# Performance work log

Measured on AMD Instinct MI355X. Metric: run time of the kernel, lower is better.

Reference implementation:

```python
import jax, jax.numpy as jnp
import numpy as np

LATENT = 128
HEADS = 4
HEAD_DIM = LATENT // HEADS
NUM_BUCKETS = 32
MAX_DISTANCE = 100000
B, N = 8, 2048


def relative_position_bucket(qpos, kpos):
    """T5-style bidirectional relative position bucketing.
    qpos, kpos: [B, N] int -> buckets [B, N, N] int32 in [0, NUM_BUCKETS).
    """
    rel = kpos[:, None, :] - qpos[:, :, None]  # [B, Nq, Nk]
    half = NUM_BUCKETS // 2
    buckets = (rel > 0).astype(jnp.int32) * half
    arel = jnp.abs(rel)
    max_exact = half // 2
    is_small = arel < max_exact
    # log-spaced buckets for larger distances
    large = max_exact + (
        jnp.log(jnp.maximum(arel, 1).astype(jnp.float32) / max_exact)
        / np.log(MAX_DISTANCE / max_exact)
        * (half - max_exact)
    ).astype(jnp.int32)
    large = jnp.minimum(large, half - 1)
    return buckets + jnp.where(is_small, arel.astype(jnp.int32), large)


def setup_inputs() -> dict:
    key = jax.random.key(0)
    ks = jax.random.split(key, 12)
    s = 0.02
    x = jax.random.normal(ks[0], (B, N, LATENT), dtype=jnp.float32)
    positions = jnp.sort(jax.random.randint(ks[1], (B, N), 0, 1000000), axis=-1)
    mask = jnp.ones((B, N), dtype=bool)
    Wq = jax.random.normal(ks[2], (LATENT, LATENT), dtype=jnp.float32) * s
    bq = jax.random.normal(ks[3], (LATENT,), dtype=jnp.float32) * s
    Wk = jax.random.normal(ks[4], (LATENT, LATENT), dtype=jnp.float32) * s
    bk = jax.random.normal(ks[5], (LATENT,), dtype=jnp.float32) * s
    Wv = jax.random.normal(ks[6], (LATENT, LATENT), dtype=jnp.float32) * s
    bv = jax.random.normal(ks[7], (LATENT,), dtype=jnp.float32) * s
    pos_w = jax.random.normal(ks[8], (NUM_BUCKETS + 1, HEADS), dtype=jnp.float32) * s
    Wo = jax.random.normal(ks[9], (LATENT, LATENT), dtype=jnp.float32) * s
    bo = jax.random.normal(ks[10], (LATENT,), dtype=jnp.float32) * s
    return {"x": x, "positions": positions, "mask": mask,
            "Wq": Wq, "bq": bq, "Wk": Wk, "bk": bk, "Wv": Wv, "bv": bv,
            "pos_w": pos_w, "Wo": Wo, "bo": bo}


def reference(x, positions, mask, Wq, bq, Wk, bk, Wv, bv, pos_w, Wo, bo):
    b, n, _ = x.shape
    # QKV projections, split heads: [b, h, n, d]
    Q = (x @ Wq + bq).reshape(b, n, HEADS, HEAD_DIM).transpose(0, 2, 1, 3)
    K = (x @ Wk + bk).reshape(b, n, HEADS, HEAD_DIM).transpose(0, 2, 1, 3)
    V = (x @ Wv + bv).reshape(b, n, HEADS, HEAD_DIM).transpose(0, 2, 1, 3)
    scores = jnp.einsum("bhqd,bhkd->bhqk", Q, K) / jnp.sqrt(
        jnp.asarray(HEAD_DIM, dtype=x.dtype))
    buckets = relative_position_bucket(positions, positions)  # [b, n, n]
    bias = pos_w[buckets]                  # [b, n, n, h]
    scores = scores + bias.transpose(0, 3, 1, 2)  # [b, h, n, n]
    scores = jnp.where(mask[:, None, None, :], scores, -jnp.inf)
    attn = jax.nn.softmax(scores, axis=-1)
    attn = jnp.nan_to_num(attn, nan=0.0)
    attended = jnp.einsum("bhqk,bhkd->bhqd", attn, V)
    attended = attended.transpose(0, 2, 1, 3).reshape(b, n, LATENT)
    return attended @ Wo + bo
```

## Files before the change

kernel.cpp:

```cpp
#include <hip/hip_runtime.h>
#include <math.h>


#define LOG2E 1.4426950408889634f
#define QKV_SCALE 0.17677669529663687f
#define QS (QKV_SCALE * LOG2E)

typedef _Float16 half8 __attribute__((ext_vector_type(8)));
typedef float ffrag __attribute__((ext_vector_type(4)));

#if __has_builtin(__builtin_amdgcn_exp2f)
#define EXP2F __builtin_amdgcn_exp2f
#else
#define EXP2F exp2f
#endif

static __device__ __forceinline__ unsigned short f16bits(float f) {
    return __builtin_bit_cast(unsigned short, (_Float16)f);
}
static __device__ __forceinline__ float h16f(unsigned int bits) {
    return (float)__builtin_bit_cast(_Float16, (unsigned short)(bits & 0xFFFFu));
}
static __device__ __forceinline__ unsigned int pk2(float a, float b) {
    return __builtin_bit_cast(unsigned int, __builtin_amdgcn_cvt_pkrtz(a, b));
}
static __device__ __forceinline__ void async_cp16(const unsigned short* g, unsigned short* l) {
    __builtin_amdgcn_global_load_lds(
        (const __attribute__((address_space(1))) unsigned int*)g,
        (__attribute__((address_space(3))) unsigned int*)l, 16, 0, 0);
}

__device__ __constant__ int SN_TAB[32] = {
     -2000000000,
    -30755, -9458, -2908, -894, -275, -84, -26,
    -7, -6, -5, -4, -3, -2, -1,
    0,
    1, 2, 3, 4, 5, 6, 7,
    8,
    27, 85, 276, 895, 2909, 9459, 30756,
    2000000000 };

__global__ __launch_bounds__(256)
void prep_seg_kernel(const float* __restrict__ Wq, const float* __restrict__ Wk,
                     const float* __restrict__ Wv, const float* __restrict__ Wo,
                     const float* __restrict__ bq, const float* __restrict__ bk,
                     const float* __restrict__ bv,
                     const int* __restrict__ positions,
                     unsigned short* __restrict__ Wt_qkv,
                     unsigned short* __restrict__ Wt_o,
                     float* __restrict__ bias_qkv,
                     unsigned int* __restrict__ segtab)
{
    if (blockIdx.x < 256) {
        const int e = blockIdx.x * 256 + threadIdx.x;
        const int m = e >> 14, r = e & 16383;
        const int c = r >> 7, k = r & 127;
        float v;
        if (m == 0)      v = Wq[k * 128 + c] * QS;
        else if (m == 1) v = Wk[k * 128 + c];
        else if (m == 2) v = Wv[k * 128 + c];
        else             v = Wo[k * 128 + c];
        if (m < 3) Wt_qkv[(m * 128 + c) * 128 + k] = f16bits(v);
        else       Wt_o[c * 128 + k] = f16bits(v);
        if (e < 128)      bias_qkv[e] = bq[e] * QS;
        else if (e < 256) bias_qkv[e] = bk[e - 128];
        else if (e < 384) bias_qkv[e] = bv[e - 256];
        return;
    }
    const int gid = (blockIdx.x - 256) * 256 + threadIdx.x;
    const int row = gid >> 5;
    const int s = gid & 31;
    const int b = row >> 11;
    const int* kp = positions + b * 2048;
    const int qp = kp[row & 2047];
    const int bucket = (s < 15) ? (15 - s) : (s == 15 ? 0 : s + 1);
    if (s == 31) { segtab[row * 32 + s] = (2048u << 16) | 31u; return; }
    const int target = qp + SN_TAB[s + 1];
    int lo = 0, hi = 2048;
    while (lo < hi) { const int mid = (lo + hi) >> 1; if (kp[mid] < target) lo = mid + 1; else hi = mid; }
    segtab[row * 32 + s] = ((unsigned)lo << 16) | (unsigned)bucket;
}

__global__ __launch_bounds__(512)
void qkv_mfma(const float* __restrict__ x, const unsigned short* __restrict__ Wt,
              const float* __restrict__ bias_qkv,
              unsigned short* __restrict__ Qb, unsigned short* __restrict__ Kb,
              unsigned short* __restrict__ Vg2)
{
    __shared__ __align__(16) unsigned short Xs[64 * 136];
    const int tid = threadIdx.x;
    const int token0 = blockIdx.x * 64;
    #pragma unroll
    for (int it = 0; it < 4; ++it) {
        const int f = tid + it * 512;
        const int row = f >> 5, k0 = (f & 31) << 2;
        const float4 xv = *(const float4*)(x + (size_t)(token0 + row) * 128 + k0);
        uint2 u;
        u.x = pk2(xv.x, xv.y);
        u.y = pk2(xv.z, xv.w);
        *(uint2*)(Xs + row * 136 + k0) = u;
    }
    __syncthreads();

    const int wave = tid >> 6, lane = tid & 63;
    const int lq = lane & 15, quad = lane >> 4;
    const int b = token0 >> 11;
    const int n0 = token0 & 2047;

    #pragma unroll
    for (int j = 0; j < 3; ++j) {
        const int ct = wave + j * 8;
        const int colbase = ct * 16;
        half8 wf[4];
        #pragma unroll
        for (int ks = 0; ks < 4; ++ks)
            wf[ks] = *(const half8*)(Wt + (colbase + lq) * 128 + ks * 32 + quad * 8);

        if (ct < 16) {
            const int c0q = colbase + quad * 4;
            const float4 bv = *(const float4*)(bias_qkv + c0q);
            #pragma unroll
            for (int msub = 0; msub < 4; ++msub) {
                ffrag acc = {bv.x, bv.y, bv.z, bv.w};
                #pragma unroll
                for (int ks = 0; ks < 4; ++ks) {
                    const half8 xf = *(const half8*)(Xs + (msub * 16 + lq) * 136 + ks * 32 + quad * 8);
                    acc = __builtin_amdgcn_mfma_f32_16x16x32_f16(wf[ks], xf, acc, 0, 0, 0);
                }
                const int n = n0 + msub * 16 + lq;
                const int c0 = c0q & 127;
                const int h = c0 >> 5, d = c0 & 31;
                const ushort4 v4 = make_ushort4(f16bits(acc[0]), f16bits(acc[1]),
                                                f16bits(acc[2]), f16bits(acc[3]));
                unsigned short* base = (ct < 8) ? Qb : Kb;
                *(ushort4*)(base + ((size_t)(b * 4 + h) * 2048 + n) * 32 + d) = v4;
            }
        } else {
            const float bias = bias_qkv[colbase + lq];
            const int c2 = colbase + lq - 256;
            const int h = c2 >> 5, d = c2 & 31;
            const size_t bhh = (size_t)(b * 4 + h);
            #pragma unroll
            for (int msub = 0; msub < 4; ++msub) {
                ffrag acc = {bias, bias, bias, bias};
                #pragma unroll
                for (int ks = 0; ks < 4; ++ks) {
                    const half8 xf = *(const half8*)(Xs + (msub * 16 + lq) * 136 + ks * 32 + quad * 8);
                    acc = __builtin_amdgcn_mfma_f32_16x16x32_f16(xf, wf[ks], acc, 0, 0, 0);
                }
                const int n = n0 + msub * 16 + quad * 4;
                const int chunk = n >> 7, kloc = n & 127;
                const int win = kloc >> 5, rem = kloc & 31;
                const int half = rem >> 4, pg = (rem >> 2) & 3;
                const int G = d * 16 + ((win * 4 + pg) ^ (d & 15));
                const size_t off = ((bhh * 16 + chunk) * 512 + G) * 8 + half * 4;
                const ushort4 v4 = make_ushort4(f16bits(acc[0]), f16bits(acc[1]),
                                                f16bits(acc[2]), f16bits(acc[3]));
                *(ushort4*)(Vg2 + off) = v4;
            }
        }
    }
}

__global__ __launch_bounds__(512, 4)
void attn_kernel(const unsigned short* __restrict__ Qb,
                 const unsigned short* __restrict__ Kb,
                 const unsigned short* __restrict__ Vg2,
                 const unsigned int* __restrict__ segtab,
                 const float* __restrict__ pos_w,
                 unsigned short* __restrict__ att)
{
    __shared__ __align__(16) unsigned short VB[2][2][4096];
    __shared__ unsigned int Sg[128 * 32];

    const int tid = threadIdx.x;
    const int wave = __builtin_amdgcn_readfirstlane(tid >> 6);
    const int lane = tid & 63;
    const int lq = lane & 15, quad = lane >> 4;
    const int group = wave >> 2, wg = wave & 3;

    const int qt = blockIdx.x & 15;
    const int bh = blockIdx.x >> 4;
    const int b = bh >> 2, h = bh & 3;
    const int q0 = qt * 128;

    const unsigned short* Kg = Kb + (size_t)bh * 2048 * 32;
    const unsigned short* Vgb = Vg2 + (size_t)bh * 65536;

    #pragma unroll
    for (int it = 0; it < 2; ++it) {
        const int g = (wg * 2 + it) * 64 + lane;
        async_cp16(Vgb + (size_t)group * 4096 + g * 8, &VB[group][0][(wg * 2 + it) * 512]);
    }

    {
        const unsigned int* src = segtab + ((size_t)b * 2048 + q0) * 32;
        #pragma unroll
        for (int it = 0; it < 2; ++it) {
            const int e4 = tid + it * 512;
            uint4 u = *(const uint4*)(src + e4 * 4);
            unsigned int* c = &u.x;
            const int row = e4 >> 3, s0 = (e4 & 7) * 4;
            const int rx = row & 31;
            #pragma unroll
            for (int i = 0; i < 4; ++i) {
                const float wf = __expf(pos_w[(c[i] & 0xFFFFu) * 4 + h]);
                Sg[row * 32 + ((s0 + i) ^ rx)] = (c[i] & 0xFFFF0000u) | f16bits(wf);
            }
        }
    }

    const int qa = q0 + wg * 32 + lq;
    const int qbn = qa + 16;
    const half8 qfa = *(const half8*)(Qb + ((size_t)bh * 2048 + qa) * 32 + quad * 8);
    const half8 qfb = *(const half8*)(Qb + ((size_t)bh * 2048 + qbn) * 32 + quad * 8);

    half8 ones;
    #pragma unroll
    for (int i = 0; i < 8; ++i) ones[i] = (_Float16)1.0f;

    ffrag o0a = {0.f,0.f,0.f,0.f}, o1a = {0.f,0.f,0.f,0.f}, o2a = {0.f,0.f,0.f,0.f};
    ffrag o0b = {0.f,0.f,0.f,0.f}, o1b = {0.f,0.f,0.f,0.f}, o2b = {0.f,0.f,0.f,0.f};
    int cura = -1, enda = 0; float wfa = 0.f;
    int curb = -1, endb = 0; float wfb = 0.f;
    const int rowa = wg * 32 + lq, rowb = rowa + 16;
    const int sga = rowa * 32, xa = rowa & 31;
    const int sgb = rowb * 32, xb = rowb & 31;

    half8 kA[4], kB[4];
    {
        const int kc0 = group * 128;
        #pragma unroll
        for (int j = 0; j < 4; ++j)
            kA[j] = *(const half8*)(Kg + (size_t)(kc0 + j * 16 + lq) * 32 + quad * 8);
    }

    __syncthreads();

    auto half_chunk = [&](const half8* karr, const unsigned short* vb, int kc, int w0) {
        #pragma unroll
        for (int dw = 0; dw < 2; ++dw) {
            const int w = w0 + dw;
            unsigned int pua[4], pub[4];
            #pragma unroll
            for (int T = 0; T < 2; ++T) {
                const half8 kf = karr[dw * 2 + T];
                ffrag sa = {0.f,0.f,0.f,0.f}, sb = {0.f,0.f,0.f,0.f};
                sa = __builtin_amdgcn_mfma_f32_16x16x32_f16(kf, qfa, sa, 0, 0, 0);
                sb = __builtin_amdgcn_mfma_f32_16x16x32_f16(kf, qfb, sb, 0, 0, 0);
                const int kidx = kc + (w * 2 + T) * 16 + quad * 4;
                float pa[4], pb[4];
                if (__builtin_expect(__any(kidx + 3 >= enda), 0)) {
                    #pragma unroll
                    for (int r = 0; r < 4; ++r) {
                        while (kidx + r >= enda) {
                            const unsigned int u = Sg[sga + ((++cura) ^ xa)];
                            enda = (int)(u >> 16); wfa = h16f(u);
                        }
                        pa[r] = EXP2F(sa[r]) * wfa;
                    }
                } else {
                    #pragma unroll
                    for (int r = 0; r < 4; ++r) pa[r] = EXP2F(sa[r]) * wfa;
                }
                if (__builtin_expect(__any(kidx + 3 >= endb), 0)) {
                    #pragma unroll
                    for (int r = 0; r < 4; ++r) {
                        while (kidx + r >= endb) {
                            const unsigned int u = Sg[sgb + ((++curb) ^ xb)];
                            endb = (int)(u >> 16); wfb = h16f(u);
                        }
                        pb[r] = EXP2F(sb[r]) * wfb;
                    }
                } else {
                    #pragma unroll
                    for (int r = 0; r < 4; ++r) pb[r] = EXP2F(sb[r]) * wfb;
                }
                pua[T * 2 + 0] = pk2(pa[0], pa[1]);
                pua[T * 2 + 1] = pk2(pa[2], pa[3]);
                pub[T * 2 + 0] = pk2(pb[0], pb[1]);
                pub[T * 2 + 1] = pk2(pb[2], pb[3]);
            }
            const int c = (w * 4 + quad) ^ lq;
            const half8 A0 = *(const half8*)(vb + (lq * 16 + c) * 8);
            const half8 A1 = *(const half8*)(vb + ((16 + lq) * 16 + c) * 8);
            const half8 Ba = __builtin_bit_cast(half8, make_int4(pua[0], pua[1], pua[2], pua[3]));
            const half8 Bb = __builtin_bit_cast(half8, make_int4(pub[0], pub[1], pub[2], pub[3]));
            o0a = __builtin_amdgcn_mfma_f32_16x16x32_f16(A0, Ba, o0a, 0, 0, 0);
            o1a = __builtin_amdgcn_mfma_f32_16x16x32_f16(A1, Ba, o1a, 0, 0, 0);
            o2a = __builtin_amdgcn_mfma_f32_16x16x32_f16(ones, Ba, o2a, 0, 0, 0);
            o0b = __builtin_amdgcn_mfma_f32_16x16x32_f16(A0, Bb, o0b, 0, 0, 0);
            o1b = __builtin_amdgcn_mfma_f32_16x16x32_f16(A1, Bb, o1b, 0, 0, 0);
            o2b = __builtin_amdgcn_mfma_f32_16x16x32_f16(ones, Bb, o2b, 0, 0, 0);
        }
    };

    for (int i = 0; i < 8; ++i) {
        const int kc = (2 * i + group) * 128;
        const unsigned short* vb = &VB[group][i & 1][0];
        if (i < 7) {
            #pragma unroll
            for (int it = 0; it < 2; ++it) {
                const int g = (wg * 2 + it) * 64 + lane;
                async_cp16(Vgb + (size_t)(2 * i + group + 2) * 4096 + g * 8,
                           &VB[group][(i + 1) & 1][(wg * 2 + it) * 512]);
            }
        }
        #pragma unroll
        for (int j = 0; j < 4; ++j)
            kB[j] = *(const half8*)(Kg + (size_t)(kc + (4 + j) * 16 + lq) * 32 + quad * 8);

        half_chunk(kA, vb, kc, 0);

        const int kcn = (i < 7) ? kc + 256 : kc;
        #pragma unroll
        for (int j = 0; j < 4; ++j)
            kA[j] = *(const half8*)(Kg + (size_t)(kcn + j * 16 + lq) * 32 + quad * 8);

        half_chunk(kB, vb, kc, 2);
        __syncthreads();
    }

    float lsa = o2a[0], lsb = o2b[0];
    float* scr = (float*)&VB[0][0][0];
    if (group == 1) {
        float* s = scr + (wg * 64 + lane) * 18;
        #pragma unroll
        for (int j = 0; j < 4; ++j) {
            s[j] = o0a[j]; s[4 + j] = o1a[j]; s[8 + j] = o0b[j]; s[12 + j] = o1b[j];
        }
        s[16] = lsa; s[17] = lsb;
    }
    __syncthreads();
    if (group == 0) {
        const float* s = scr + (wg * 64 + lane) * 18;
        #pragma unroll
        for (int j = 0; j < 4; ++j) {
            o0a[j] += s[j]; o1a[j] += s[4 + j]; o0b[j] += s[8 + j]; o1b[j] += s[12 + j];
        }
        lsa += s[16]; lsb += s[17];
        const float inva = 1.0f / lsa;
        const float invb = 1.0f / lsb;

        unsigned short* da = att + (size_t)(b * 2048 + qa) * 128 + h * 32 + quad * 4;
        uint2 r0, r1;
        r0.x = pk2(o0a[0] * inva, o0a[1] * inva);
        r0.y = pk2(o0a[2] * inva, o0a[3] * inva);
        r1.x = pk2(o1a[0] * inva, o1a[1] * inva);
        r1.y = pk2(o1a[2] * inva, o1a[3] * inva);
        *(uint2*)da = r0;
        *(uint2*)(da + 16) = r1;

        unsigned short* db = att + (size_t)(b * 2048 + qbn) * 128 + h * 32 + quad * 4;
        r0.x = pk2(o0b[0] * invb, o0b[1] * invb);
        r0.y = pk2(o0b[2] * invb, o0b[3] * invb);
        r1.x = pk2(o1b[0] * invb, o1b[1] * invb);
        r1.y = pk2(o1b[2] * invb, o1b[3] * invb);
        *(uint2*)db = r0;
        *(uint2*)(db + 16) = r1;
    }
}

__global__ __launch_bounds__(512)
void out_mfma(const unsigned short* __restrict__ att,
              const unsigned short* __restrict__ Wt_o,
              const float* __restrict__ bo, float* __restrict__ out)
{
    __shared__ __align__(16) unsigned short Xs[64 * 136];
    const int tid = threadIdx.x;
    const int token0 = blockIdx.x * 64;
    #pragma unroll
    for (int it = 0; it < 2; ++it) {
        const int f = tid + it * 512;
        const int row = f >> 4, k0 = (f & 15) << 3;
        const uint4 v = *(const uint4*)(att + (size_t)(token0 + row) * 128 + k0);
        *(uint4*)(Xs + row * 136 + k0) = v;
    }
    __syncthreads();

    const int wave = tid >> 6, lane = tid & 63;
    const int lq = lane & 15, quad = lane >> 4;
    const int colbase = wave * 16;

    half8 wf[4];
    #pragma unroll
    for (int ks = 0; ks < 4; ++ks)
        wf[ks] = *(const half8*)(Wt_o + (colbase + lq) * 128 + ks * 32 + quad * 8);
    const float4 bv = *(const float4*)(bo + colbase + quad * 4);

    #pragma unroll
    for (int msub = 0; msub < 4; ++msub) {
        ffrag acc = {bv.x, bv.y, bv.z, bv.w};
        #pragma unroll
        for (int ks = 0; ks < 4; ++ks) {
            const half8 xf = *(const half8*)(Xs + (msub * 16 + lq) * 136 + ks * 32 + quad * 8);
            acc = __builtin_amdgcn_mfma_f32_16x16x32_f16(wf[ks], xf, acc, 0, 0, 0);
        }
        const int c0 = colbase + quad * 4;
        *(float4*)(out + (size_t)(token0 + msub * 16 + lq) * 128 + c0) =
            make_float4(acc[0], acc[1], acc[2], acc[3]);
    }
}

extern "C" void kernel_launch(void* const* d_in, const int* in_sizes, int n_in,
                              void* d_out, int out_size, void* d_ws, size_t ws_size,
                              hipStream_t stream)
{
    const float* x         = (const float*)d_in[0];
    const int*   positions = (const int*)d_in[1];
    const float* Wq = (const float*)d_in[3];
    const float* bq = (const float*)d_in[4];
    const float* Wk = (const float*)d_in[5];
    const float* bk = (const float*)d_in[6];
    const float* Wv = (const float*)d_in[7];
    const float* bv = (const float*)d_in[8];
    const float* pw = (const float*)d_in[9];
    const float* Wo = (const float*)d_in[10];
    const float* bo = (const float*)d_in[11];
    float* out = (float*)d_out;

    unsigned short* Qb  = (unsigned short*)d_ws;
    unsigned short* Kb  = Qb + 2097152;
    unsigned short* Vg2 = Kb + 2097152;
    unsigned short* att = Vg2 + 2097152;
    unsigned int* segtab = (unsigned int*)(att + 2097152);
    unsigned short* Wt_qkv = (unsigned short*)(segtab + 524288);
    unsigned short* Wt_o = Wt_qkv + 49152;
    float* bias_qkv = (float*)(Wt_o + 16384);

    prep_seg_kernel<<<2304, 256, 0, stream>>>(Wq, Wk, Wv, Wo, bq, bk, bv, positions,
                                              Wt_qkv, Wt_o, bias_qkv, segtab);
    qkv_mfma<<<256, 512, 0, stream>>>(x, Wt_qkv, bias_qkv, Qb, Kb, Vg2);
    attn_kernel<<<512, 512, 0, stream>>>(Qb, Kb, Vg2, segtab, pw, att);
    out_mfma<<<256, 512, 0, stream>>>(att, Wt_o, bo, out);
}
```

Baseline: 149.3 us.

## Split attention into 64-query tiles with four-way key-group parallelism

The attention kernel now processes 64 query rows per block instead of 128 and splits the keys across four wave groups instead of two, using 64-key chunks. The grid grows to 1024 blocks and launch bounds ask for more resident blocks. The V projection writes a matching 64-key swizzled layout, and the final reduction combines partial outputs from three groups through shared memory. The goal is more parallel work per CU and better latency hiding, at the cost of more per-block setup, repeated segment-table and pos_w exponent work, and a larger cross-group reduction.

```diff
diff --git a/kernel.cpp b/kernel.cpp
--- a/kernel.cpp
+++ b/kernel.cpp
@@ -149,11 +149,12 @@
                     acc = __builtin_amdgcn_mfma_f32_16x16x32_f16(xf, wf[ks], acc, 0, 0, 0);
                 }
                 const int n = n0 + msub * 16 + quad * 4;
-                const int chunk = n >> 7, kloc = n & 127;
-                const int win = kloc >> 5, rem = kloc & 31;
-                const int half = rem >> 4, pg = (rem >> 2) & 3;
-                const int G = d * 16 + ((win * 4 + pg) ^ (d & 15));
-                const size_t off = ((bhh * 16 + chunk) * 512 + G) * 8 + half * 4;
+                const int chunk = n >> 6;
+                const int kloc = n & 63;
+                const int win = kloc >> 5;
+                const int halfq = (kloc >> 4) & 1;
+                const int slot = d * 8 + (((win << 2) | quad) ^ (d & 7));
+                const size_t off = (((size_t)bhh * 32 + chunk) * 256 + slot) * 8 + halfq * 4;
                 const ushort4 v4 = make_ushort4(f16bits(acc[0]), f16bits(acc[1]),
                                                 f16bits(acc[2]), f16bits(acc[3]));
                 *(ushort4*)(Vg2 + off) = v4;
@@ -162,7 +163,7 @@
     }
 }
 
-__global__ __launch_bounds__(512, 4)
+__global__ __launch_bounds__(512, 8)
 void attn_kernel(const unsigned short* __restrict__ Qb,
                  const unsigned short* __restrict__ Kb,
                  const unsigned short* __restrict__ Vg2,
@@ -170,19 +171,19 @@
                  const float* __restrict__ pos_w,
                  unsigned short* __restrict__ att)
 {
-    __shared__ __align__(16) unsigned short VB[2][2][4096];
-    __shared__ unsigned int Sg[128 * 32];
+    __shared__ __align__(16) unsigned short VB[4][2][2048];
+    __shared__ unsigned int Sg[64 * 32];
 
     const int tid = threadIdx.x;
     const int wave = __builtin_amdgcn_readfirstlane(tid >> 6);
     const int lane = tid & 63;
     const int lq = lane & 15, quad = lane >> 4;
-    const int group = wave >> 2, wg = wave & 3;
-
-    const int qt = blockIdx.x & 15;
-    const int bh = blockIdx.x >> 4;
+    const int group = wave >> 1, wg = wave & 1;
+
+    const int qt = blockIdx.x & 31;
+    const int bh = blockIdx.x >> 5;
     const int b = bh >> 2, h = bh & 3;
-    const int q0 = qt * 128;
+    const int q0 = qt * 64;
 
     const unsigned short* Kg = Kb + (size_t)bh * 2048 * 32;
     const unsigned short* Vgb = Vg2 + (size_t)bh * 65536;
@@ -190,23 +191,20 @@
     #pragma unroll
     for (int it = 0; it < 2; ++it) {
         const int g = (wg * 2 + it) * 64 + lane;
-        async_cp16(Vgb + (size_t)group * 4096 + g * 8, &VB[group][0][(wg * 2 + it) * 512]);
+        async_cp16(Vgb + (size_t)group * 2048 + g * 8, &VB[group][0][(wg * 2 + it) * 512]);
     }
 
     {
         const unsigned int* src = segtab + ((size_t)b * 2048 + q0) * 32;
-        #pragma unroll
-        for (int it = 0; it < 2; ++it) {
-            const int e4 = tid + it * 512;
-            uint4 u = *(const uint4*)(src + e4 * 4);
-            unsigned int* c = &u.x;
-            const int row = e4 >> 3, s0 = (e4 & 7) * 4;
-            const int rx = row & 31;
-            #pragma unroll
-            for (int i = 0; i < 4; ++i) {
-                const float wf = __expf(pos_w[(c[i] & 0xFFFFu) * 4 + h]);
-                Sg[row * 32 + ((s0 + i) ^ rx)] = (c[i] & 0xFFFF0000u) | f16bits(wf);
-            }
+        const int e4 = tid;
+        uint4 u = *(const uint4*)(src + e4 * 4);
+        unsigned int* c = &u.x;
+        const int row = e4 >> 3, s0 = (e4 & 7) * 4;
+        const int rx = row & 31;
+        #pragma unroll
+        for (int i = 0; i < 4; ++i) {
+            const float wf = __expf(pos_w[(c[i] & 0xFFFFu) * 4 + h]);
+            Sg[row * 32 + ((s0 + i) ^ rx)] = (c[i] & 0xFFFF0000u) | f16bits(wf);
         }
     }
 
@@ -229,7 +227,7 @@
 
     half8 kA[4], kB[4];
     {
-        const int kc0 = group * 128;
+        const int kc0 = group * 64;
         #pragma unroll
         for (int j = 0; j < 4; ++j)
             kA[j] = *(const half8*)(Kg + (size_t)(kc0 + j * 16 + lq) * 32 + quad * 8);
@@ -237,10 +235,9 @@
 
     __syncthreads();
 
-    auto half_chunk = [&](const half8* karr, const unsigned short* vb, int kc, int w0) {
+    auto do_chunk = [&](const half8* karr, const unsigned short* vb, int kc) {
         #pragma unroll
         for (int dw = 0; dw < 2; ++dw) {
-            const int w = w0 + dw;
             unsigned int pua[4], pub[4];
             #pragma unroll
             for (int T = 0; T < 2; ++T) {
@@ -248,7 +245,7 @@
                 ffrag sa = {0.f,0.f,0.f,0.f}, sb = {0.f,0.f,0.f,0.f};
                 sa = __builtin_amdgcn_mfma_f32_16x16x32_f16(kf, qfa, sa, 0, 0, 0);
                 sb = __builtin_amdgcn_mfma_f32_16x16x32_f16(kf, qfb, sb, 0, 0, 0);
-                const int kidx = kc + (w * 2 + T) * 16 + quad * 4;
+                const int kidx = kc + (dw * 2 + T) * 16 + quad * 4;
                 float pa[4], pb[4];
                 if (__builtin_expect(__any(kidx + 3 >= enda), 0)) {
                     #pragma unroll
@@ -281,9 +278,9 @@
                 pub[T * 2 + 0] = pk2(pb[0], pb[1]);
                 pub[T * 2 + 1] = pk2(pb[2], pb[3]);
             }
-            const int c = (w * 4 + quad) ^ lq;
-            const half8 A0 = *(const half8*)(vb + (lq * 16 + c) * 8);
-            const half8 A1 = *(const half8*)(vb + ((16 + lq) * 16 + c) * 8);
+            const int s = ((dw << 2) | quad) ^ (lq & 7);
+            const half8 A0 = *(const half8*)(vb + (lq * 8 + s) * 8);
+            const half8 A1 = *(const half8*)(vb + ((16 + lq) * 8 + s) * 8);
             const half8 Ba = __builtin_bit_cast(half8, make_int4(pua[0], pua[1], pua[2], pua[3]));
             const half8 Bb = __builtin_bit_cast(half8, make_int4(pub[0], pub[1], pub[2], pub[3]));
             o0a = __builtin_amdgcn_mfma_f32_16x16x32_f16(A0, Ba, o0a, 0, 0, 0);
@@ -295,50 +292,61 @@
         }
     };
 
-    for (int i = 0; i < 8; ++i) {
-        const int kc = (2 * i + group) * 128;
-        const unsigned short* vb = &VB[group][i & 1][0];
-        if (i < 7) {
+    for (int ii = 0; ii < 4; ++ii) {
+        {
+            const int kc = ((2 * ii) * 4 + group) * 64;
             #pragma unroll
             for (int it = 0; it < 2; ++it) {
                 const int g = (wg * 2 + it) * 64 + lane;
-                async_cp16(Vgb + (size_t)(2 * i + group + 2) * 4096 + g * 8,
-                           &VB[group][(i + 1) & 1][(wg * 2 + it) * 512]);
-            }
-        }
-        #pragma unroll
-        for (int j = 0; j < 4; ++j)
-            kB[j] = *(const half8*)(Kg + (size_t)(kc + (4 + j) * 16 + lq) * 32 + quad * 8);
-
-        half_chunk(kA, vb, kc, 0);
-
-        const int kcn = (i < 7) ? kc + 256 : kc;
-        #pragma unroll
-        for (int j = 0; j < 4; ++j)
-            kA[j] = *(const half8*)(Kg + (size_t)(kcn + j * 16 + lq) * 32 + quad * 8);
-
-        half_chunk(kB, vb, kc, 2);
-        __syncthreads();
+                async_cp16(Vgb + (size_t)((2 * ii + 1) * 4 + group) * 2048 + g * 8,
+                           &VB[group][1][(wg * 2 + it) * 512]);
+            }
+            #pragma unroll
+            for (int j = 0; j < 4; ++j)
+                kB[j] = *(const half8*)(Kg + (size_t)(kc + 256 + j * 16 + lq) * 32 + quad * 8);
+            do_chunk(kA, &VB[group][0][0], kc);
+            __syncthreads();
+        }
+        {
+            const int kc = ((2 * ii + 1) * 4 + group) * 64;
+            if (ii < 3) {
+                #pragma unroll
+                for (int it = 0; it < 2; ++it) {
+                    const int g = (wg * 2 + it) * 64 + lane;
+                    async_cp16(Vgb + (size_t)((2 * ii + 2) * 4 + group) * 2048 + g * 8,
+                               &VB[group][0][(wg * 2 + it) * 512]);
+                }
+            }
+            const int kcn = (ii < 3) ? kc + 256 : kc;
+            #pragma unroll
+            for (int j = 0; j < 4; ++j)
+                kA[j] = *(const half8*)(Kg + (size_t)(kcn + j * 16 + lq) * 32 + quad * 8);
+            do_chunk(kB, &VB[group][1][0], kc);
+            __syncthreads();
+        }
     }
 
     float lsa = o2a[0], lsb = o2b[0];
     float* scr = (float*)&VB[0][0][0];
-    if (group == 1) {
-        float* s = scr + (wg * 64 + lane) * 18;
+    if (group != 0) {
+        float* sp = scr + (((group - 1) * 2 + wg) * 64 + lane) * 18;
         #pragma unroll
         for (int j = 0; j < 4; ++j) {
-            s[j] = o0a[j]; s[4 + j] = o1a[j]; s[8 + j] = o0b[j]; s[12 + j] = o1b[j];
-        }
-        s[16] = lsa; s[17] = lsb;
+            sp[j] = o0a[j]; sp[4 + j] = o1a[j]; sp[8 + j] = o0b[j]; sp[12 + j] = o1b[j];
+        }
+        sp[16] = lsa; sp[17] = lsb;
     }
     __syncthreads();
     if (group == 0) {
-        const float* s = scr + (wg * 64 + lane) * 18;
-        #pragma unroll
-        for (int j = 0; j < 4; ++j) {
-            o0a[j] += s[j]; o1a[j] += s[4 + j]; o0b[j] += s[8 + j]; o1b[j] += s[12 + j];
-        }
-        lsa += s[16]; lsb += s[17];
+        #pragma unroll
+        for (int g = 0; g < 3; ++g) {
+            const float* sp = scr + ((g * 2 + wg) * 64 + lane) * 18;
+            #pragma unroll
+            for (int j = 0; j < 4; ++j) {
+                o0a[j] += sp[j]; o1a[j] += sp[4 + j]; o0b[j] += sp[8 + j]; o1b[j] += sp[12 + j];
+            }
+            lsa += sp[16]; lsb += sp[17];
+        }
         const float inva = 1.0f / lsa;
         const float invb = 1.0f / lsb;
 
@@ -431,6 +439,6 @@
     prep_seg_kernel<<<2304, 256, 0, stream>>>(Wq, Wk, Wv, Wo, bq, bk, bv, positions,
                                               Wt_qkv, Wt_o, bias_qkv, segtab);
     qkv_mfma<<<256, 512, 0, stream>>>(x, Wt_qkv, bias_qkv, Qb, Kb, Vg2);
-    attn_kernel<<<512, 512, 0, stream>>>(Qb, Kb, Vg2, segtab, pw, att);
+    attn_kernel<<<1024, 512, 0, stream>>>(Qb, Kb, Vg2, segtab, pw, att);
     out_mfma<<<256, 512, 0, stream>>>(att, Wt_o, bo, out);
 }
```

Measured after the change: 295.8 us. 1.98x slower.
